# Kernel tuning notes

Measured on AMD Instinct MI355X. Metric: run time of the kernel, lower is better.

The kernel has to match this reference:

```python
import jax, jax.numpy as jnp
import numpy as np

DIM = 384
HEAD_DIM = 32
NUM_HEADS = DIM // HEAD_DIM
SCALE = HEAD_DIM ** -0.5


def setup_inputs() -> dict:
    key = jax.random.key(0)
    k1, k2, k3, k4 = jax.random.split(key, 4)
    x = jax.random.normal(k1, (8, DIM, 32, 32), dtype=jnp.float32)
    # torch nn.Linear stores weight as [out_features, in_features]
    W_qkv = jax.random.normal(k2, (3 * DIM, DIM), dtype=jnp.float32) * (DIM ** -0.5)
    W_proj = jax.random.normal(k3, (DIM, DIM), dtype=jnp.float32) * (DIM ** -0.5)
    b_proj = jax.random.normal(k4, (DIM,), dtype=jnp.float32) * 0.01
    return {"x": x, "W_qkv": W_qkv, "W_proj": W_proj, "b_proj": b_proj}


def reference(x, W_qkv, W_proj, b_proj):
    B, C, H, W = x.shape
    N = H * W
    # flatten spatial -> tokens: (B, N, C)
    xt = x.reshape(B, C, N).transpose(0, 2, 1)
    # qkv projection (no bias): (B, N, 3C)
    qkv = jnp.einsum('bnc,oc->bno', xt, W_qkv)
    qkv = qkv.reshape(B, N, 3, NUM_HEADS, HEAD_DIM).transpose(2, 0, 3, 1, 4)
    q, k, v = qkv[0], qkv[1], qkv[2]  # each (B, h, N, d)
    attn = jnp.einsum('bhnd,bhmd->bhnm', q * SCALE, k)  # (B, h, N, N)
    attn = jax.nn.softmax(attn, axis=-1)
    out = jnp.einsum('bhnm,bhmd->bhnd', attn, v)  # (B, h, N, d)
    out = out.transpose(0, 2, 1, 3).reshape(B, N, C)
    out = jnp.einsum('bnc,oc->bno', out, W_proj) + b_proj
    # back to (B, C, H, W)
    return out.transpose(0, 2, 1).reshape(B, C, H, W)
```

## Files before the change

### kernel.cpp

```cpp
#include <hip/hip_runtime.h>

#define DIM   384
#define HD    32
#define NH    12
#define NT    1024
#define BATCH 8
#define C2 0.2550347244197545f
#define M2 11.541560327111707f


typedef short shortx8 __attribute__((ext_vector_type(8)));
typedef float floatx4 __attribute__((ext_vector_type(4)));

static __device__ __forceinline__ unsigned short f2bf(float f) {
    unsigned int u = __float_as_uint(f);
    u += 0x7fffu + ((u >> 16) & 1u);
    return (unsigned short)(u >> 16);
}

__global__ __launch_bounds__(256) void k_transpose(const float* __restrict__ x,
                                                   unsigned short* __restrict__ xtf) {
    __shared__ float t[32][33];
    const int b = blockIdx.z, kstep = blockIdx.y, n0 = blockIdx.x * 32;
    const int tid = threadIdx.x;
    const int tx = tid & 31, ty = tid >> 5;
    const float* xb = x + ((size_t)b * DIM + kstep * 32) * NT + n0;
#pragma unroll
    for (int i = 0; i < 4; i++)
        t[ty + 8 * i][tx] = xb[(size_t)(ty + 8 * i) * NT + tx];
    __syncthreads();
    const int mtl = tid >> 7, kq = (tid >> 5) & 3, rem = tid & 31;
    const int mrow = rem >> 1, krH = rem & 1;
    ushort4 p;
    p.x = f2bf(t[kq * 8 + krH * 4 + 0][mtl * 16 + mrow]);
    p.y = f2bf(t[kq * 8 + krH * 4 + 1][mtl * 16 + mrow]);
    p.z = f2bf(t[kq * 8 + krH * 4 + 2][mtl * 16 + mrow]);
    p.w = f2bf(t[kq * 8 + krH * 4 + 3][mtl * 16 + mrow]);
    const size_t mtile = ((size_t)b * 1024 + n0) / 16 + mtl;
    const size_t off = ((mtile * 12 + kstep) * 4 + kq) * 128 + mrow * 8 + krH * 4;
    *(ushort4*)(xtf + off) = p;
}

#define NCQ 110592
__global__ __launch_bounds__(256) void k_castw(const float* __restrict__ wq,
                                               const float* __restrict__ wp,
                                               unsigned short* __restrict__ wqf,
                                               unsigned short* __restrict__ wpf) {
    const int tid = blockIdx.x * 256 + threadIdx.x;
    const float* src; unsigned short* dst; int ci;
    if (tid < NCQ) { ci = tid; src = wq; dst = wqf; }
    else           { ci = tid - NCQ; src = wp; dst = wpf; }
    const int krH = ci & 1, orow = (ci >> 1) & 15, quad = (ci >> 5) & 3;
    const int t2 = ci >> 7, kstep = t2 % 12, ntile = t2 / 12;
    const int row = ntile * 16 + orow, col = kstep * 32 + quad * 8 + krH * 4;
    const float4 v = *(const float4*)(src + (size_t)row * DIM + col);
    ushort4 p;
    p.x = f2bf(v.x); p.y = f2bf(v.y); p.z = f2bf(v.z); p.w = f2bf(v.w);
    *(ushort4*)(dst + (size_t)ci * 4) = p;
}

__global__ __launch_bounds__(256) void k_qkv(const unsigned short* __restrict__ xtf,
                                             const unsigned short* __restrict__ wqf,
                                             unsigned short* __restrict__ qb,
                                             unsigned short* __restrict__ kb,
                                             unsigned short* __restrict__ vt) {
    const int lane = threadIdx.x & 63, w = threadIdx.x >> 6;
    const int quad = lane >> 4, l16 = lane & 15;
    const int m0 = blockIdx.x * 128 + (w & 1) * 64;
    const int n0 = blockIdx.y * 128 + (w >> 1) * 64;
    floatx4 acc[4][4] = {};
    const unsigned short* abase = xtf + ((size_t)(m0 >> 4) * 12 * 4 + quad) * 128 + l16 * 8;
    const unsigned short* bbase = wqf + ((size_t)(n0 >> 4) * 12 * 4 + quad) * 128 + l16 * 8;
    for (int ks = 0; ks < 12; ks++) {
        shortx8 a[4], b[4];
#pragma unroll
        for (int s = 0; s < 4; s++) a[s] = *(const shortx8*)(abase + s * 6144 + ks * 512);
#pragma unroll
        for (int s = 0; s < 4; s++) b[s] = *(const shortx8*)(bbase + s * 6144 + ks * 512);
#pragma unroll
        for (int sm = 0; sm < 4; sm++)
#pragma unroll
            for (int sn = 0; sn < 4; sn++)
                acc[sm][sn] = __builtin_amdgcn_mfma_f32_16x16x32_bf16(a[sm], b[sn], acc[sm][sn], 0, 0, 0);
    }
    const int bi = m0 >> 10;
#pragma unroll
    for (int sn = 0; sn < 4; sn++) {
        const int o = n0 + sn * 16 + l16;
        const int which = (o >= 2 * DIM) ? 2 : (o >= DIM ? 1 : 0);
        const int rem = o - which * DIM;
        const int h = rem >> 5, d = rem & 31;
        const int hi = bi * NH + h;
#pragma unroll
        for (int sm = 0; sm < 4; sm++) {
#pragma unroll
            for (int r = 0; r < 4; r++) {
                const int n = (m0 + sm * 16 + quad * 4 + r) & 1023;
                const unsigned short val = f2bf(acc[sm][sn][r]);
                if (which == 0)      qb[((size_t)hi * NT + n) * HD + d] = val;
                else if (which == 1) kb[((size_t)hi * NT + n) * HD + d] = val;
                else                 vt[((size_t)hi * HD + d) * NT + n] = val;
            }
        }
    }
}

__global__ __launch_bounds__(256) void k_attn(const unsigned short* __restrict__ qb,
                                              const unsigned short* __restrict__ kb,
                                              const unsigned short* __restrict__ vt,
                                              unsigned short* __restrict__ aoutf) {
    const int lane = threadIdx.x & 63, w = threadIdx.x >> 6;
    const int quad = lane >> 4, l16 = lane & 15;
    const int g = blockIdx.x & 7, j = blockIdx.x >> 3;
    const int hi = g * 12 + j % 12;
    const int q0 = ((j / 12) * 4 + w) * 32;
    const unsigned short* Q = qb + (size_t)hi * NT * HD;
    const unsigned short* K = kb + (size_t)hi * NT * HD;
    const unsigned short* V = vt + (size_t)hi * HD * NT;

    const shortx8 qfA = *(const shortx8*)(Q + (size_t)(q0 + l16) * HD + quad * 8);
    const shortx8 qfB = *(const shortx8*)(Q + (size_t)(q0 + 16 + l16) * HD + quad * 8);
    const int krow = (l16 >> 2) * 8 + (l16 & 3);
    const shortx8 ones = {16256, 16256, 16256, 16256, 16256, 16256, 16256, 16256};
    floatx4 oloA = {}, ohiA = {}, dsA = {};
    floatx4 oloB = {}, ohiB = {}, dsB = {};
    const floatx4 zero = {};

    for (int kt = 0; kt < NT; kt += 32) {
        const shortx8 kf0 = *(const shortx8*)(K + (size_t)(kt + krow) * HD + quad * 8);
        const shortx8 kf1 = *(const shortx8*)(K + (size_t)(kt + krow + 4) * HD + quad * 8);
        const shortx8 vlo = *(const shortx8*)(V + (size_t)l16 * NT + kt + quad * 8);
        const shortx8 vhi = *(const shortx8*)(V + (size_t)(16 + l16) * NT + kt + quad * 8);
        const floatx4 sA0 = __builtin_amdgcn_mfma_f32_16x16x32_bf16(kf0, qfA, zero, 0, 0, 0);
        const floatx4 sA1 = __builtin_amdgcn_mfma_f32_16x16x32_bf16(kf1, qfA, zero, 0, 0, 0);
        const floatx4 sB0 = __builtin_amdgcn_mfma_f32_16x16x32_bf16(kf0, qfB, zero, 0, 0, 0);
        const floatx4 sB1 = __builtin_amdgcn_mfma_f32_16x16x32_bf16(kf1, qfB, zero, 0, 0, 0);
        shortx8 pfA, pfB;
#pragma unroll
        for (int r = 0; r < 4; r++) {
            pfA[r]     = (short)f2bf(__builtin_amdgcn_exp2f(fmaf(sA0[r], C2, -M2)));
            pfA[4 + r] = (short)f2bf(__builtin_amdgcn_exp2f(fmaf(sA1[r], C2, -M2)));
            pfB[r]     = (short)f2bf(__builtin_amdgcn_exp2f(fmaf(sB0[r], C2, -M2)));
            pfB[4 + r] = (short)f2bf(__builtin_amdgcn_exp2f(fmaf(sB1[r], C2, -M2)));
        }
        oloA = __builtin_amdgcn_mfma_f32_16x16x32_bf16(pfA, vlo, oloA, 0, 0, 0);
        ohiA = __builtin_amdgcn_mfma_f32_16x16x32_bf16(pfA, vhi, ohiA, 0, 0, 0);
        dsA  = __builtin_amdgcn_mfma_f32_16x16x32_bf16(pfA, ones, dsA, 0, 0, 0);
        oloB = __builtin_amdgcn_mfma_f32_16x16x32_bf16(pfB, vlo, oloB, 0, 0, 0);
        ohiB = __builtin_amdgcn_mfma_f32_16x16x32_bf16(pfB, vhi, ohiB, 0, 0, 0);
        dsB  = __builtin_amdgcn_mfma_f32_16x16x32_bf16(pfB, ones, dsB, 0, 0, 0);
    }
    const int bi = hi / NH, h = hi % NH;
    const size_t mt0 = (size_t)bi * 64 + (q0 >> 4);
    const int kqlo = l16 >> 3, kr = l16 & 7;
    unsigned short* pA = aoutf + (mt0 * 12 + h) * 512 + kr;
    unsigned short* pB = aoutf + ((mt0 + 1) * 12 + h) * 512 + kr;
#pragma unroll
    for (int r = 0; r < 4; r++) {
        const int mrow8 = (quad * 4 + r) * 8;
        const float invA = 1.0f / dsA[r], invB = 1.0f / dsB[r];
        pA[kqlo * 128 + mrow8]       = f2bf(oloA[r] * invA);
        pA[(2 + kqlo) * 128 + mrow8] = f2bf(ohiA[r] * invA);
        pB[kqlo * 128 + mrow8]       = f2bf(oloB[r] * invB);
        pB[(2 + kqlo) * 128 + mrow8] = f2bf(ohiB[r] * invB);
    }
}

__global__ __launch_bounds__(256) void k_proj(const unsigned short* __restrict__ aoutf,
                                              const unsigned short* __restrict__ wpf,
                                              const float* __restrict__ bias,
                                              float* __restrict__ out) {
    const int lane = threadIdx.x & 63, w = threadIdx.x >> 6;
    const int quad = lane >> 4, l16 = lane & 15;
    const int m0 = blockIdx.x * 128 + (w & 1) * 64;
    const int n0 = blockIdx.y * 128 + (w >> 1) * 64;
    floatx4 acc[4][4] = {};
    const unsigned short* abase = aoutf + ((size_t)(m0 >> 4) * 12 * 4 + quad) * 128 + l16 * 8;
    const unsigned short* bbase = wpf + ((size_t)(n0 >> 4) * 12 * 4 + quad) * 128 + l16 * 8;
    for (int ks = 0; ks < 12; ks++) {
        shortx8 a[4], b[4];
#pragma unroll
        for (int s = 0; s < 4; s++) a[s] = *(const shortx8*)(abase + s * 6144 + ks * 512);
#pragma unroll
        for (int s = 0; s < 4; s++) b[s] = *(const shortx8*)(bbase + s * 6144 + ks * 512);
#pragma unroll
        for (int sm = 0; sm < 4; sm++)
#pragma unroll
            for (int sn = 0; sn < 4; sn++)
                acc[sm][sn] = __builtin_amdgcn_mfma_f32_16x16x32_bf16(a[sm], b[sn], acc[sm][sn], 0, 0, 0);
    }
    const int bi = m0 >> 10;
#pragma unroll
    for (int sn = 0; sn < 4; sn++) {
        const int o = n0 + sn * 16 + l16;
        const float bv = bias[o];
        float* orow = out + ((size_t)bi * DIM + o) * NT;
#pragma unroll
        for (int sm = 0; sm < 4; sm++) {
            const int nb = (m0 + sm * 16 + quad * 4) & 1023;
            float4 pack;
            pack.x = acc[sm][sn][0] + bv;
            pack.y = acc[sm][sn][1] + bv;
            pack.z = acc[sm][sn][2] + bv;
            pack.w = acc[sm][sn][3] + bv;
            *(float4*)(orow + nb) = pack;
        }
    }
}

extern "C" void kernel_launch(void* const* d_in, const int* in_sizes, int n_in,
                              void* d_out, int out_size, void* d_ws, size_t ws_size,
                              hipStream_t stream) {
    const float* x     = (const float*)d_in[0];
    const float* wqkv  = (const float*)d_in[1];
    const float* wproj = (const float*)d_in[2];
    const float* bias  = (const float*)d_in[3];
    float* out = (float*)d_out;

    unsigned short* xtf  = (unsigned short*)d_ws;
    unsigned short* qb   = xtf + 3145728;
    unsigned short* kb   = qb + 3145728;
    unsigned short* vt   = kb + 3145728;
    unsigned short* wqf  = vt + 3145728;
    unsigned short* wpf  = wqf + 442368;
    unsigned short* aoutf = xtf;

    k_transpose<<<dim3(32, 12, 8), 256, 0, stream>>>(x, xtf);
    k_castw<<<576, 256, 0, stream>>>(wqkv, wproj, wqf, wpf);
    k_qkv<<<dim3(64, 9), 256, 0, stream>>>(xtf, wqf, qb, kb, vt);
    k_attn<<<768, 256, 0, stream>>>(qb, kb, vt, aoutf);
    k_proj<<<dim3(64, 3), 256, 0, stream>>>(aoutf, wpf, bias, out);
}
```

Before: 149.7 us.

## Merge prep kernels, prefetch GEMM fragments, stage attention K/V via LDS

Merges the transpose and weight-cast kernels into one launch, saving a kernel launch. Software-prefetches the next k-step's A/B fragments into registers in the QKV and projection GEMMs. In attention, each wave loads one K/V fragment per tile into double-buffered LDS with global_load_lds, so four waves share one load instead of each loading all four, and packs exp results with packed bf16 conversion. This adds a block-wide barrier every tile and more register pressure in the GEMMs.

```diff
diff --git a/kernel.cpp b/kernel.cpp
--- a/kernel.cpp
+++ b/kernel.cpp
@@ -1,4 +1,5 @@
 #include <hip/hip_runtime.h>
+#include <hip/hip_bf16.h>
 
 #define DIM   384
 #define HD    32
@@ -12,51 +13,57 @@
 typedef short shortx8 __attribute__((ext_vector_type(8)));
 typedef float floatx4 __attribute__((ext_vector_type(4)));
 
+#define GLD_LDS(gp, lp) \
+    __builtin_amdgcn_global_load_lds((__attribute__((address_space(1))) const void*)(gp), \
+                                     (__attribute__((address_space(3))) void*)(lp), 16, 0, 0)
+
 static __device__ __forceinline__ unsigned short f2bf(float f) {
     unsigned int u = __float_as_uint(f);
     u += 0x7fffu + ((u >> 16) & 1u);
     return (unsigned short)(u >> 16);
 }
 
-__global__ __launch_bounds__(256) void k_transpose(const float* __restrict__ x,
-                                                   unsigned short* __restrict__ xtf) {
-    __shared__ float t[32][33];
-    const int b = blockIdx.z, kstep = blockIdx.y, n0 = blockIdx.x * 32;
-    const int tid = threadIdx.x;
-    const int tx = tid & 31, ty = tid >> 5;
-    const float* xb = x + ((size_t)b * DIM + kstep * 32) * NT + n0;
-#pragma unroll
-    for (int i = 0; i < 4; i++)
-        t[ty + 8 * i][tx] = xb[(size_t)(ty + 8 * i) * NT + tx];
-    __syncthreads();
-    const int mtl = tid >> 7, kq = (tid >> 5) & 3, rem = tid & 31;
-    const int mrow = rem >> 1, krH = rem & 1;
-    ushort4 p;
-    p.x = f2bf(t[kq * 8 + krH * 4 + 0][mtl * 16 + mrow]);
-    p.y = f2bf(t[kq * 8 + krH * 4 + 1][mtl * 16 + mrow]);
-    p.z = f2bf(t[kq * 8 + krH * 4 + 2][mtl * 16 + mrow]);
-    p.w = f2bf(t[kq * 8 + krH * 4 + 3][mtl * 16 + mrow]);
-    const size_t mtile = ((size_t)b * 1024 + n0) / 16 + mtl;
-    const size_t off = ((mtile * 12 + kstep) * 4 + kq) * 128 + mrow * 8 + krH * 4;
-    *(ushort4*)(xtf + off) = p;
-}
-
-#define NCQ 110592
-__global__ __launch_bounds__(256) void k_castw(const float* __restrict__ wq,
-                                               const float* __restrict__ wp,
-                                               unsigned short* __restrict__ wqf,
-                                               unsigned short* __restrict__ wpf) {
-    const int tid = blockIdx.x * 256 + threadIdx.x;
-    const float* src; unsigned short* dst; int ci;
-    if (tid < NCQ) { ci = tid; src = wq; dst = wqf; }
-    else           { ci = tid - NCQ; src = wp; dst = wpf; }
-    const int krH = ci & 1, orow = (ci >> 1) & 15, quad = (ci >> 5) & 3;
-    const int t2 = ci >> 7, kstep = t2 % 12, ntile = t2 / 12;
-    const int row = ntile * 16 + orow, col = kstep * 32 + quad * 8 + krH * 4;
-    const float4 v = *(const float4*)(src + (size_t)row * DIM + col);
-    ushort4 p;
-    p.x = f2bf(v.x); p.y = f2bf(v.y); p.z = f2bf(v.z); p.w = f2bf(v.w);
-    *(ushort4*)(dst + (size_t)ci * 4) = p;
+__global__ __launch_bounds__(256) void k_pre(const float* __restrict__ x,
+                                             const float* __restrict__ wq,
+                                             const float* __restrict__ wp,
+                                             unsigned short* __restrict__ xtf,
+                                             unsigned short* __restrict__ wqf,
+                                             unsigned short* __restrict__ wpf) {
+    const int bid = blockIdx.x;
+    if (bid < 3072) {
+        __shared__ float t[32][33];
+        const int xb_ = bid & 31, kstep = (bid >> 5) % 12, b = bid / 384;
+        const int n0 = xb_ * 32;
+        const int tid = threadIdx.x;
+        const int tx = tid & 31, ty = tid >> 5;
+        const float* xb = x + ((size_t)b * DIM + kstep * 32) * NT + n0;
+#pragma unroll
+        for (int i = 0; i < 4; i++)
+            t[ty + 8 * i][tx] = xb[(size_t)(ty + 8 * i) * NT + tx];
+        __syncthreads();
+        const int mtl = tid >> 7, kq = (tid >> 5) & 3, rem = tid & 31;
+        const int mrow = rem >> 1, krH = rem & 1;
+        ushort4 p;
+        p.x = f2bf(t[kq * 8 + krH * 4 + 0][mtl * 16 + mrow]);
+        p.y = f2bf(t[kq * 8 + krH * 4 + 1][mtl * 16 + mrow]);
+        p.z = f2bf(t[kq * 8 + krH * 4 + 2][mtl * 16 + mrow]);
+        p.w = f2bf(t[kq * 8 + krH * 4 + 3][mtl * 16 + mrow]);
+        const size_t mtile = ((size_t)b * 1024 + n0) / 16 + mtl;
+        const size_t off = ((mtile * 12 + kstep) * 4 + kq) * 128 + mrow * 8 + krH * 4;
+        *(ushort4*)(xtf + off) = p;
+    } else {
+        const int tid = (bid - 3072) * 256 + threadIdx.x;
+        const float* src; unsigned short* dst; int ci;
+        if (tid < 110592) { ci = tid; src = wq; dst = wqf; }
+        else              { ci = tid - 110592; src = wp; dst = wpf; }
+        const int krH = ci & 1, orow = (ci >> 1) & 15, quad = (ci >> 5) & 3;
+        const int t2 = ci >> 7, kstep = t2 % 12, ntile = t2 / 12;
+        const int row = ntile * 16 + orow, col = kstep * 32 + quad * 8 + krH * 4;
+        const float4 v = *(const float4*)(src + (size_t)row * DIM + col);
+        ushort4 p;
+        p.x = f2bf(v.x); p.y = f2bf(v.y); p.z = f2bf(v.z); p.w = f2bf(v.w);
+        *(ushort4*)(dst + (size_t)ci * 4) = p;
+    }
 }
 
 __global__ __launch_bounds__(256) void k_qkv(const unsigned short* __restrict__ xtf,
@@ -71,17 +78,27 @@
     floatx4 acc[4][4] = {};
     const unsigned short* abase = xtf + ((size_t)(m0 >> 4) * 12 * 4 + quad) * 128 + l16 * 8;
     const unsigned short* bbase = wqf + ((size_t)(n0 >> 4) * 12 * 4 + quad) * 128 + l16 * 8;
+    shortx8 a[4], b[4], a2[4], b2[4];
+#pragma unroll
+    for (int s = 0; s < 4; s++) {
+        a[s] = *(const shortx8*)(abase + s * 6144);
+        b[s] = *(const shortx8*)(bbase + s * 6144);
+    }
     for (int ks = 0; ks < 12; ks++) {
-        shortx8 a[4], b[4];
-#pragma unroll
-        for (int s = 0; s < 4; s++) a[s] = *(const shortx8*)(abase + s * 6144 + ks * 512);
-#pragma unroll
-        for (int s = 0; s < 4; s++) b[s] = *(const shortx8*)(bbase + s * 6144 + ks * 512);
+        if (ks < 11) {
+#pragma unroll
+            for (int s = 0; s < 4; s++) {
+                a2[s] = *(const shortx8*)(abase + s * 6144 + (ks + 1) * 512);
+                b2[s] = *(const shortx8*)(bbase + s * 6144 + (ks + 1) * 512);
+            }
+        }
 #pragma unroll
         for (int sm = 0; sm < 4; sm++)
 #pragma unroll
             for (int sn = 0; sn < 4; sn++)
                 acc[sm][sn] = __builtin_amdgcn_mfma_f32_16x16x32_bf16(a[sm], b[sn], acc[sm][sn], 0, 0, 0);
+#pragma unroll
+        for (int s = 0; s < 4; s++) { a[s] = a2[s]; b[s] = b2[s]; }
     }
     const int bi = m0 >> 10;
 #pragma unroll
@@ -109,6 +126,7 @@
                                               const unsigned short* __restrict__ kb,
                                               const unsigned short* __restrict__ vt,
                                               unsigned short* __restrict__ aoutf) {
+    __shared__ __align__(16) unsigned short frag[2][4][512];
     const int lane = threadIdx.x & 63, w = threadIdx.x >> 6;
     const int quad = lane >> 4, l16 = lane & 15;
     const int g = blockIdx.x & 7, j = blockIdx.x >> 3;
@@ -121,48 +139,67 @@
     const shortx8 qfA = *(const shortx8*)(Q + (size_t)(q0 + l16) * HD + quad * 8);
     const shortx8 qfB = *(const shortx8*)(Q + (size_t)(q0 + 16 + l16) * HD + quad * 8);
     const int krow = (l16 >> 2) * 8 + (l16 & 3);
+    const unsigned short* gsrc0;
+    if (w == 0)      gsrc0 = K + (size_t)krow * HD + quad * 8;
+    else if (w == 1) gsrc0 = K + (size_t)(krow + 4) * HD + quad * 8;
+    else if (w == 2) gsrc0 = V + (size_t)l16 * NT + quad * 8;
+    else             gsrc0 = V + (size_t)(16 + l16) * NT + quad * 8;
+    const int gstep = (w < 2) ? 32 * HD : 32;
+
     const shortx8 ones = {16256, 16256, 16256, 16256, 16256, 16256, 16256, 16256};
     floatx4 oloA = {}, ohiA = {}, dsA = {};
     floatx4 oloB = {}, ohiB = {}, dsB = {};
     const floatx4 zero = {};
 
-    for (int kt = 0; kt < NT; kt += 32) {
-        const shortx8 kf0 = *(const shortx8*)(K + (size_t)(kt + krow) * HD + quad * 8);
-        const shortx8 kf1 = *(const shortx8*)(K + (size_t)(kt + krow + 4) * HD + quad * 8);
-        const shortx8 vlo = *(const shortx8*)(V + (size_t)l16 * NT + kt + quad * 8);
-        const shortx8 vhi = *(const shortx8*)(V + (size_t)(16 + l16) * NT + kt + quad * 8);
+    GLD_LDS(gsrc0, &frag[0][w][0]);
+    __syncthreads();
+
+    for (int t = 0; t < 32; t++) {
+        if (t < 31) GLD_LDS(gsrc0 + (size_t)(t + 1) * gstep, &frag[(t + 1) & 1][w][0]);
+        const unsigned short* fb = &frag[t & 1][0][0];
+        const shortx8 kf0 = *(const shortx8*)(fb + 0 * 512 + lane * 8);
+        const shortx8 kf1 = *(const shortx8*)(fb + 1 * 512 + lane * 8);
+        const shortx8 vlo = *(const shortx8*)(fb + 2 * 512 + lane * 8);
+        const shortx8 vhi = *(const shortx8*)(fb + 3 * 512 + lane * 8);
         const floatx4 sA0 = __builtin_amdgcn_mfma_f32_16x16x32_bf16(kf0, qfA, zero, 0, 0, 0);
         const floatx4 sA1 = __builtin_amdgcn_mfma_f32_16x16x32_bf16(kf1, qfA, zero, 0, 0, 0);
         const floatx4 sB0 = __builtin_amdgcn_mfma_f32_16x16x32_bf16(kf0, qfB, zero, 0, 0, 0);
         const floatx4 sB1 = __builtin_amdgcn_mfma_f32_16x16x32_bf16(kf1, qfB, zero, 0, 0, 0);
-        shortx8 pfA, pfB;
+        float eA[8], eB[8];
 #pragma unroll
         for (int r = 0; r < 4; r++) {
-            pfA[r]     = (short)f2bf(__builtin_amdgcn_exp2f(fmaf(sA0[r], C2, -M2)));
-            pfA[4 + r] = (short)f2bf(__builtin_amdgcn_exp2f(fmaf(sA1[r], C2, -M2)));
-            pfB[r]     = (short)f2bf(__builtin_amdgcn_exp2f(fmaf(sB0[r], C2, -M2)));
-            pfB[4 + r] = (short)f2bf(__builtin_amdgcn_exp2f(fmaf(sB1[r], C2, -M2)));
-        }
-        oloA = __builtin_amdgcn_mfma_f32_16x16x32_bf16(pfA, vlo, oloA, 0, 0, 0);
-        ohiA = __builtin_amdgcn_mfma_f32_16x16x32_bf16(pfA, vhi, ohiA, 0, 0, 0);
-        dsA  = __builtin_amdgcn_mfma_f32_16x16x32_bf16(pfA, ones, dsA, 0, 0, 0);
-        oloB = __builtin_amdgcn_mfma_f32_16x16x32_bf16(pfB, vlo, oloB, 0, 0, 0);
-        ohiB = __builtin_amdgcn_mfma_f32_16x16x32_bf16(pfB, vhi, ohiB, 0, 0, 0);
-        dsB  = __builtin_amdgcn_mfma_f32_16x16x32_bf16(pfB, ones, dsB, 0, 0, 0);
+            eA[r]     = __builtin_amdgcn_exp2f(fmaf(sA0[r], C2, -M2));
+            eA[4 + r] = __builtin_amdgcn_exp2f(fmaf(sA1[r], C2, -M2));
+            eB[r]     = __builtin_amdgcn_exp2f(fmaf(sB0[r], C2, -M2));
+            eB[4 + r] = __builtin_amdgcn_exp2f(fmaf(sB1[r], C2, -M2));
+        }
+        union { shortx8 s8; __hip_bfloat162 h[4]; } pA, pB;
+#pragma unroll
+        for (int i = 0; i < 4; i++) {
+            pA.h[i] = __float22bfloat162_rn(make_float2(eA[2 * i], eA[2 * i + 1]));
+            pB.h[i] = __float22bfloat162_rn(make_float2(eB[2 * i], eB[2 * i + 1]));
+        }
+        oloA = __builtin_amdgcn_mfma_f32_16x16x32_bf16(pA.s8, vlo, oloA, 0, 0, 0);
+        ohiA = __builtin_amdgcn_mfma_f32_16x16x32_bf16(pA.s8, vhi, ohiA, 0, 0, 0);
+        dsA  = __builtin_amdgcn_mfma_f32_16x16x32_bf16(pA.s8, ones, dsA, 0, 0, 0);
+        oloB = __builtin_amdgcn_mfma_f32_16x16x32_bf16(pB.s8, vlo, oloB, 0, 0, 0);
+        ohiB = __builtin_amdgcn_mfma_f32_16x16x32_bf16(pB.s8, vhi, ohiB, 0, 0, 0);
+        dsB  = __builtin_amdgcn_mfma_f32_16x16x32_bf16(pB.s8, ones, dsB, 0, 0, 0);
+        __syncthreads();
     }
     const int bi = hi / NH, h = hi % NH;
     const size_t mt0 = (size_t)bi * 64 + (q0 >> 4);
     const int kqlo = l16 >> 3, kr = l16 & 7;
-    unsigned short* pA = aoutf + (mt0 * 12 + h) * 512 + kr;
-    unsigned short* pB = aoutf + ((mt0 + 1) * 12 + h) * 512 + kr;
+    unsigned short* pAp = aoutf + (mt0 * 12 + h) * 512 + kr;
+    unsigned short* pBp = aoutf + ((mt0 + 1) * 12 + h) * 512 + kr;
 #pragma unroll
     for (int r = 0; r < 4; r++) {
         const int mrow8 = (quad * 4 + r) * 8;
         const float invA = 1.0f / dsA[r], invB = 1.0f / dsB[r];
-        pA[kqlo * 128 + mrow8]       = f2bf(oloA[r] * invA);
-        pA[(2 + kqlo) * 128 + mrow8] = f2bf(ohiA[r] * invA);
-        pB[kqlo * 128 + mrow8]       = f2bf(oloB[r] * invB);
-        pB[(2 + kqlo) * 128 + mrow8] = f2bf(ohiB[r] * invB);
+        pAp[kqlo * 128 + mrow8]       = f2bf(oloA[r] * invA);
+        pAp[(2 + kqlo) * 128 + mrow8] = f2bf(ohiA[r] * invA);
+        pBp[kqlo * 128 + mrow8]       = f2bf(oloB[r] * invB);
+        pBp[(2 + kqlo) * 128 + mrow8] = f2bf(ohiB[r] * invB);
     }
 }
 
@@ -177,17 +214,27 @@
     floatx4 acc[4][4] = {};
     const unsigned short* abase = aoutf + ((size_t)(m0 >> 4) * 12 * 4 + quad) * 128 + l16 * 8;
     const unsigned short* bbase = wpf + ((size_t)(n0 >> 4) * 12 * 4 + quad) * 128 + l16 * 8;
+    shortx8 a[4], b[4], a2[4], b2[4];
+#pragma unroll
+    for (int s = 0; s < 4; s++) {
+        a[s] = *(const shortx8*)(abase + s * 6144);
+        b[s] = *(const shortx8*)(bbase + s * 6144);
+    }
     for (int ks = 0; ks < 12; ks++) {
-        shortx8 a[4], b[4];
-#pragma unroll
-        for (int s = 0; s < 4; s++) a[s] = *(const shortx8*)(abase + s * 6144 + ks * 512);
-#pragma unroll
-        for (int s = 0; s < 4; s++) b[s] = *(const shortx8*)(bbase + s * 6144 + ks * 512);
+        if (ks < 11) {
+#pragma unroll
+            for (int s = 0; s < 4; s++) {
+                a2[s] = *(const shortx8*)(abase + s * 6144 + (ks + 1) * 512);
+                b2[s] = *(const shortx8*)(bbase + s * 6144 + (ks + 1) * 512);
+            }
+        }
 #pragma unroll
         for (int sm = 0; sm < 4; sm++)
 #pragma unroll
             for (int sn = 0; sn < 4; sn++)
                 acc[sm][sn] = __builtin_amdgcn_mfma_f32_16x16x32_bf16(a[sm], b[sn], acc[sm][sn], 0, 0, 0);
+#pragma unroll
+        for (int s = 0; s < 4; s++) { a[s] = a2[s]; b[s] = b2[s]; }
     }
     const int bi = m0 >> 10;
 #pragma unroll
@@ -225,8 +272,7 @@
     unsigned short* wpf  = wqf + 442368;
     unsigned short* aoutf = xtf;
 
-    k_transpose<<<dim3(32, 12, 8), 256, 0, stream>>>(x, xtf);
-    k_castw<<<576, 256, 0, stream>>>(wqkv, wproj, wqf, wpf);
+    k_pre<<<3648, 256, 0, stream>>>(x, wqkv, wproj, xtf, wqf, wpf);
     k_qkv<<<dim3(64, 9), 256, 0, stream>>>(xtf, wqf, qb, kb, vt);
     k_attn<<<768, 256, 0, stream>>>(qb, kb, vt, aoutf);
     k_proj<<<dim3(64, 3), 256, 0, stream>>>(aoutf, wpf, bias, out);
```

After: 128.6 us. -14.1%, faster.
